# Optimization experiments

Measured on AMD Instinct MI355X. Metric: run time of the kernel, lower is better.

The kernel has to match this reference:

```python
import jax, jax.numpy as jnp
import numpy as np

N = 50000      # nodes
E = 800000     # edges (avg degree 16)
DIN = 128
HID = 128
OUT = 10       # classes
G = 64         # graphs in batch


def setup_inputs() -> dict:
    key = jax.random.key(0)
    ks = jax.random.split(key, 10)
    x = jax.random.normal(ks[0], (N, DIN), dtype=jnp.float32)
    edge_index = jax.random.randint(ks[1], (2, E), 0, N, dtype=jnp.int32)
    edge_weight = jax.random.uniform(ks[2], (E,), dtype=jnp.float32)
    batch = jnp.sort(jax.random.randint(ks[3], (N,), 0, G, dtype=jnp.int32))
    W1 = jax.random.normal(ks[4], (DIN, HID), dtype=jnp.float32) / np.sqrt(DIN)
    b1 = jnp.zeros((HID,), dtype=jnp.float32)
    W2 = jax.random.normal(ks[5], (HID, HID), dtype=jnp.float32) / np.sqrt(HID)
    b2 = jnp.zeros((HID,), dtype=jnp.float32)
    W3 = jax.random.normal(ks[6], (HID, OUT), dtype=jnp.float32) / np.sqrt(HID)
    b3 = jnp.zeros((OUT,), dtype=jnp.float32)
    return {"x": x, "edge_index": edge_index, "edge_weight": edge_weight,
            "batch": batch, "W1": W1, "b1": b1, "W2": W2, "b2": b2,
            "W3": W3, "b3": b3}


def _gcn_norm(edge_index, edge_weight, n_nodes):
    # PyG gcn_norm: add self-loops with weight 1, D^-1/2 (A+I) D^-1/2
    loop = jnp.arange(n_nodes, dtype=edge_index.dtype)
    src = jnp.concatenate([edge_index[0], loop])
    dst = jnp.concatenate([edge_index[1], loop])
    w = jnp.concatenate([edge_weight, jnp.ones((n_nodes,), edge_weight.dtype)])
    deg = jax.ops.segment_sum(w, dst, num_segments=n_nodes)
    dinv = jnp.where(deg > 0, jax.lax.rsqrt(deg), 0.0)
    norm = dinv[src] * w * dinv[dst]
    return src, dst, norm


def _gcn_conv(x, W, b, src, dst, norm, n_nodes):
    h = x @ W                                      # [N, F] dense transform
    msg = norm[:, None] * h[src]                   # gather + scale  [E+N, F]
    out = jax.ops.segment_sum(msg, dst, num_segments=n_nodes)  # scatter-add
    return out + b


def reference(x, edge_index, edge_weight, batch, W1, b1, W2, b2, W3, b3):
    src, dst, norm = _gcn_norm(edge_index, edge_weight, N)
    h = jax.nn.relu(_gcn_conv(x, W1, b1, src, dst, norm, N))
    h = jax.nn.relu(_gcn_conv(h, W2, b2, src, dst, norm, N))
    h = _gcn_conv(h, W3, b3, src, dst, norm, N)    # [N, OUT]
    # global_mean_pool over graph ids
    sums = jax.ops.segment_sum(h, batch, num_segments=G)          # [G, OUT]
    cnts = jax.ops.segment_sum(jnp.ones((N,), h.dtype), batch, num_segments=G)
    pooled = sums / jnp.maximum(cnts, 1.0)[:, None]
    return jax.nn.log_softmax(pooled, axis=1)
```

## Files before the change

### kernel.cpp

```cpp
#include <hip/hip_runtime.h>
#include <math.h>

#define NN 50000
#define EE 800000
#define GG 64
#define FD 128
#define OUTD 10
#define NB 49
#define GB 782
#define BB 196
#define NBU 196
#define NBK 128
#define CH 6250

typedef __attribute__((ext_vector_type(8))) short s8v;
typedef __attribute__((ext_vector_type(4))) float f4v;

static __device__ inline unsigned short f2b(float f) {
    unsigned int u = __float_as_uint(f);
    return (unsigned short)((u + 0x7FFFu + ((u >> 16) & 1u)) >> 16);
}


__global__ void k_prep(const float* __restrict__ W1, const float* __restrict__ W2,
                       unsigned short* __restrict__ Wt1, unsigned short* __restrict__ Wt2,
                       int* __restrict__ bflag) {
    int i = blockIdx.x * blockDim.x + threadIdx.x;
    if (i < FD * FD) {
        int nn = i >> 7, k = i & 127;
        Wt1[i] = f2b(W1[k * FD + nn]);
        Wt2[i] = f2b(W2[k * FD + nn]);
    }
    if (i < NB) bflag[i] = 0;
}


static __device__ inline void gemm_f32in_body(int bid, const float* __restrict__ A,
        const unsigned short* __restrict__ Wt, unsigned short* __restrict__ out, int n) {
    int tid = threadIdx.x;
    int wave = tid >> 6, lane = tid & 63;
    int quad = lane >> 4, c16 = lane & 15;
    int rowbase = bid * 64 + wave * 16;
    int rowA = rowbase + c16;
    if (rowA >= n) rowA = n - 1;
    f4v acc[8];
    #pragma unroll
    for (int t = 0; t < 8; ++t) acc[t] = (f4v){0.f, 0.f, 0.f, 0.f};
    #pragma unroll
    for (int k0 = 0; k0 < 128; k0 += 32) {
        const float* ap = A + (size_t)rowA * FD + k0 + quad * 8;
        float4 a0 = *(const float4*)ap;
        float4 a1 = *(const float4*)(ap + 4);
        s8v a;
        a[0] = (short)f2b(a0.x); a[1] = (short)f2b(a0.y);
        a[2] = (short)f2b(a0.z); a[3] = (short)f2b(a0.w);
        a[4] = (short)f2b(a1.x); a[5] = (short)f2b(a1.y);
        a[6] = (short)f2b(a1.z); a[7] = (short)f2b(a1.w);
        #pragma unroll
        for (int t = 0; t < 8; ++t) {
            s8v b = *(const s8v*)(Wt + (size_t)(t * 16 + c16) * FD + k0 + quad * 8);
            acc[t] = __builtin_amdgcn_mfma_f32_16x16x32_bf16(a, b, acc[t], 0, 0, 0);
        }
    }
    #pragma unroll
    for (int t = 0; t < 8; ++t) {
        #pragma unroll
        for (int r = 0; r < 4; ++r) {
            int row = rowbase + quad * 4 + r;
            if (row < n) out[(size_t)row * FD + t * 16 + c16] = f2b(acc[t][r]);
        }
    }
}

__global__ __launch_bounds__(256) void k_megaA(const float* __restrict__ x,
        const unsigned short* __restrict__ Wt1, unsigned short* __restrict__ hA,
        const int* __restrict__ dst, int* __restrict__ cnt2d,
        const int* __restrict__ batch, int* __restrict__ gstart) {
    int b = blockIdx.x;
    int tid = threadIdx.x;
    if (b < GB) {
        gemm_f32in_body(b, x, Wt1, hA, NN);
    } else if (b < GB + NBK) {
        __shared__ unsigned hist[NBU];
        int blk = b - GB;
        if (tid < NBU) hist[tid] = 0;
        __syncthreads();
        int e0 = blk * CH;
        for (int e = e0 + tid; e < e0 + CH; e += 256)
            atomicAdd(&hist[(unsigned)dst[e] >> 8], 1u);
        __syncthreads();
        if (tid < NBU) cnt2d[blk * NBU + tid] = (int)hist[tid];
    } else {
        int i = (b - GB - NBK) * 256 + tid;
        if (i < NN) {
            int bb = batch[i];
            int bp = (i == 0) ? -1 : batch[i - 1];
            for (int g = bp + 1; g <= bb; ++g) gstart[g] = i;
            if (i == NN - 1)
                for (int g = bb + 1; g <= GG; ++g) gstart[g] = NN;
        }
    }
}


__global__ __launch_bounds__(256) void k_bscan(int* __restrict__ cnt2d,
        int* __restrict__ bucketbase) {
    __shared__ int colsum[NBU];
    int tid = threadIdx.x;
    if (tid < NBU) {
        int run = 0;
        for (int blk = 0; blk < NBK; ++blk) {
            int idx = blk * NBU + tid;
            int t = cnt2d[idx];
            cnt2d[idx] = run;
            run += t;
        }
        colsum[tid] = run;
    }
    __syncthreads();
    if (tid == 0) {
        int run = 0;
        for (int b = 0; b < NBU; ++b) {
            bucketbase[b] = run;
            run += colsum[b];
        }
        bucketbase[NBU] = run;
    }
}


__global__ __launch_bounds__(256) void k_scatter(const int* __restrict__ src,
        const int* __restrict__ dst, const float* __restrict__ ew,
        const int* __restrict__ off2d, const int* __restrict__ bucketbase,
        uint2* __restrict__ rec) {
    __shared__ unsigned cur[NBU];
    int tid = threadIdx.x;
    int blk = blockIdx.x;
    if (tid < NBU) cur[tid] = (unsigned)(bucketbase[tid] + off2d[blk * NBU + tid]);
    __syncthreads();
    int e0 = blk * CH;
    for (int e = e0 + tid; e < e0 + CH; e += 256) {
        int d = dst[e];
        unsigned bkt = (unsigned)d >> 8;
        unsigned pos = atomicAdd(&cur[bkt], 1u);
        rec[pos] = make_uint2(((unsigned)(d & 255) << 16) | (unsigned)src[e],
                              __float_as_uint(ew[e]));
    }
}


__global__ __launch_bounds__(1024) void k_rank(const uint2* __restrict__ rec,
        const int* __restrict__ bucketbase, unsigned short* __restrict__ rankb,
        int* __restrict__ cnt_g, float* __restrict__ wdeg_g) {
    __shared__ unsigned cntS[256];
    __shared__ float wdegS[256];
    int b = blockIdx.x;
    int tid = threadIdx.x;
    if (tid < 256) { cntS[tid] = 0; wdegS[tid] = 0.0f; }
    __syncthreads();
    int beg = bucketbase[b], end = bucketbase[b + 1];
    for (int s = beg + tid; s < end; s += 1024) {
        uint2 r = rec[s];
        unsigned dl = r.x >> 16;
        unsigned old = atomicAdd(&cntS[dl], 1u);
        rankb[s] = (unsigned short)old;
        atomicAdd(&wdegS[dl], __uint_as_float(r.y));
    }
    __syncthreads();
    if (tid < 256) {
        int node = b * 256 + tid;
        if (node < NN) {
            cnt_g[node] = (int)cntS[tid];
            wdeg_g[node] = wdegS[tid];
        }
    }
}


__global__ __launch_bounds__(1024) void k_scan(const int* __restrict__ cnt_g,
        const float* __restrict__ wdeg_g, int* __restrict__ rowptr,
        float* __restrict__ dinv, uint2* __restrict__ ent,
        int* __restrict__ bsum, int* __restrict__ bflag, int n) {
    __shared__ int wtot[16];
    __shared__ int sbase_sh;
    int tid = threadIdx.x;
    int bid = blockIdx.x;
    int i = bid * 1024 + tid;
    int lane = tid & 63, wv = tid >> 6;

    int v_edges = 0, rowlen = 0;
    float di = 0.0f;
    if (i < n) {
        v_edges = cnt_g[i];
        float deg = wdeg_g[i] + 1.0f;
        di = 1.0f / sqrtf(deg);
        dinv[i] = di;
        rowlen = v_edges + 1;
    }
    int s = rowlen;
    #pragma unroll
    for (int off = 1; off < 64; off <<= 1) {
        int u = __shfl_up(s, off, 64);
        if (lane >= off) s += u;
    }
    if (lane == 63) wtot[wv] = s;
    __syncthreads();

    int btot = 0;
    #pragma unroll
    for (int j = 0; j < 16; ++j) btot += wtot[j];
    if (tid == 0) {
        bsum[bid] = btot;
        __hip_atomic_store(&bflag[bid], 1, __ATOMIC_RELEASE, __HIP_MEMORY_SCOPE_AGENT);
    }
    if (tid < 64) {
        int acc = 0;
        if (tid < bid) {
            while (__hip_atomic_load(&bflag[tid], __ATOMIC_ACQUIRE,
                                     __HIP_MEMORY_SCOPE_AGENT) == 0) {}
            acc = bsum[tid];
        }
        #pragma unroll
        for (int off = 32; off >= 1; off >>= 1) acc += __shfl_xor(acc, off, 64);
        if (tid == 0) sbase_sh = acc;
    }
    __syncthreads();
    int base = sbase_sh;

    int wpre = 0;
    for (int j = 0; j < wv; ++j) wpre += wtot[j];
    if (i < n) {
        int r = base + wpre + (s - rowlen);
        rowptr[i] = r;
        ent[r + v_edges] = make_uint2((unsigned)i, __float_as_uint(di * di));
    }
    if (bid == NB - 1 && tid == 0) rowptr[n] = base + btot;
}


__global__ __launch_bounds__(1024) void k_fill2(const uint2* __restrict__ rec,
        const unsigned short* __restrict__ rankb, const int* __restrict__ bucketbase,
        const int* __restrict__ rowptr, const float* __restrict__ dinv,
        uint2* __restrict__ ent) {
    int b = blockIdx.x;
    int tid = threadIdx.x;
    int beg = bucketbase[b], end = bucketbase[b + 1];
    for (int s = beg + tid; s < end; s += 1024) {
        uint2 r = rec[s];
        unsigned sn = r.x & 0xFFFFu;
        int d = (b << 8) | (int)(r.x >> 16);
        int pos = rowptr[d] + (int)rankb[s];
        float val = dinv[sn] * __uint_as_float(r.y) * dinv[d];
        ent[pos] = make_uint2(sn, __float_as_uint(val));
    }
}


__global__ __launch_bounds__(256) void k_gemm_bf(const unsigned short* __restrict__ A,
        const unsigned short* __restrict__ Wt, unsigned short* __restrict__ out, int n) {
    int tid = threadIdx.x;
    int wave = tid >> 6, lane = tid & 63;
    int quad = lane >> 4, c16 = lane & 15;
    int rowbase = blockIdx.x * 64 + wave * 16;
    int rowA = rowbase + c16;
    if (rowA >= n) rowA = n - 1;
    f4v acc[8];
    #pragma unroll
    for (int t = 0; t < 8; ++t) acc[t] = (f4v){0.f, 0.f, 0.f, 0.f};
    #pragma unroll
    for (int k0 = 0; k0 < 128; k0 += 32) {
        s8v a = *(const s8v*)(A + (size_t)rowA * FD + k0 + quad * 8);
        #pragma unroll
        for (int t = 0; t < 8; ++t) {
            s8v b = *(const s8v*)(Wt + (size_t)(t * 16 + c16) * FD + k0 + quad * 8);
            acc[t] = __builtin_amdgcn_mfma_f32_16x16x32_bf16(a, b, acc[t], 0, 0, 0);
        }
    }
    #pragma unroll
    for (int t = 0; t < 8; ++t) {
        #pragma unroll
        for (int r = 0; r < 4; ++r) {
            int row = rowbase + quad * 4 + r;
            if (row < n) out[(size_t)row * FD + t * 16 + c16] = f2b(acc[t][r]);
        }
    }
}

__global__ void k_gemm10(const unsigned short* __restrict__ A, const float* __restrict__ W,
                         float* __restrict__ out, int n) {
    __shared__ float Ws[FD * OUTD];
    int tid = threadIdx.x;
    for (int i = tid; i < FD * OUTD; i += blockDim.x) Ws[i] = W[i];
    __syncthreads();
    int i = blockIdx.x * blockDim.x + tid;
    if (i >= n) return;
    float acc[OUTD];
    #pragma unroll
    for (int c = 0; c < OUTD; ++c) acc[c] = 0.0f;
    const unsigned short* a = A + (size_t)i * FD;
    for (int k0 = 0; k0 < FD; k0 += 8) {
        uint4 t = *(const uint4*)(a + k0);
        float av[8];
        av[0] = __uint_as_float(t.x << 16); av[1] = __uint_as_float(t.x & 0xFFFF0000u);
        av[2] = __uint_as_float(t.y << 16); av[3] = __uint_as_float(t.y & 0xFFFF0000u);
        av[4] = __uint_as_float(t.z << 16); av[5] = __uint_as_float(t.z & 0xFFFF0000u);
        av[6] = __uint_as_float(t.w << 16); av[7] = __uint_as_float(t.w & 0xFFFF0000u);
        #pragma unroll
        for (int j = 0; j < 8; ++j)
            #pragma unroll
            for (int c = 0; c < OUTD; ++c) acc[c] += av[j] * Ws[(k0 + j) * OUTD + c];
    }
    float* o = out + (size_t)i * OUTD;
    #pragma unroll
    for (int c = 0; c < OUTD; ++c) o[c] = acc[c];
}

__global__ __launch_bounds__(256) void k_spmm_bf(const int* __restrict__ rowptr,
        const uint2* __restrict__ ent, const unsigned short* __restrict__ tin,
        const float* __restrict__ bias, unsigned short* __restrict__ out,
        int n, int dorelu) {
    int w = (blockIdx.x * blockDim.x + threadIdx.x) >> 6;
    int lane = threadIdx.x & 63;
    if (w >= n) return;
    int c = lane & 15, g = lane >> 4;
    int beg = rowptr[w], end = rowptr[w + 1];
    float acc[8];
    #pragma unroll
    for (int j = 0; j < 8; ++j) acc[j] = 0.0f;
    for (int e0 = beg; e0 < end; e0 += 16) {
        uint2 en[4];
        uint4 t[4];
        #pragma unroll
        for (int u = 0; u < 4; ++u) {
            int e = e0 + 4 * u + g;
            en[u] = (e < end) ? ent[e] : make_uint2(0u, 0u);
        }
        #pragma unroll
        for (int u = 0; u < 4; ++u)
            t[u] = *(const uint4*)(tin + (size_t)en[u].x * FD + c * 8);
        #pragma unroll
        for (int u = 0; u < 4; ++u) {
            float v = __uint_as_float(en[u].y);
            acc[0] += v * __uint_as_float(t[u].x << 16);
            acc[1] += v * __uint_as_float(t[u].x & 0xFFFF0000u);
            acc[2] += v * __uint_as_float(t[u].y << 16);
            acc[3] += v * __uint_as_float(t[u].y & 0xFFFF0000u);
            acc[4] += v * __uint_as_float(t[u].z << 16);
            acc[5] += v * __uint_as_float(t[u].z & 0xFFFF0000u);
            acc[6] += v * __uint_as_float(t[u].w << 16);
            acc[7] += v * __uint_as_float(t[u].w & 0xFFFF0000u);
        }
    }
    #pragma unroll
    for (int j = 0; j < 8; ++j) {
        acc[j] += __shfl_xor(acc[j], 16, 64);
        acc[j] += __shfl_xor(acc[j], 32, 64);
    }
    if (g == 0) {
        uint4 r;
        float o[8];
        #pragma unroll
        for (int j = 0; j < 8; ++j) {
            float x = acc[j] + bias[c * 8 + j];
            o[j] = dorelu ? fmaxf(x, 0.0f) : x;
        }
        r.x = (unsigned)f2b(o[0]) | ((unsigned)f2b(o[1]) << 16);
        r.y = (unsigned)f2b(o[2]) | ((unsigned)f2b(o[3]) << 16);
        r.z = (unsigned)f2b(o[4]) | ((unsigned)f2b(o[5]) << 16);
        r.w = (unsigned)f2b(o[6]) | ((unsigned)f2b(o[7]) << 16);
        *(uint4*)(out + (size_t)w * FD + c * 8) = r;
    }
}

__global__ void k_spmm10(const int* __restrict__ rowptr, const uint2* __restrict__ ent,
        const float* __restrict__ tin, const float* __restrict__ bias,
        float* __restrict__ out, int n) {
    int t = blockIdx.x * blockDim.x + threadIdx.x;
    int node = t / OUTD;
    int c = t - node * OUTD;
    if (node >= n) return;
    int beg = rowptr[node], end = rowptr[node + 1];
    float acc = 0.0f;
    for (int e = beg; e < end; ++e) {
        uint2 en = ent[e];
        acc += __uint_as_float(en.y) * tin[(size_t)en.x * OUTD + c];
    }
    out[(size_t)node * OUTD + c] = acc + bias[c];
}


__global__ __launch_bounds__(256) void k_poolfin(const float* __restrict__ h,
        const int* __restrict__ gstart, float* __restrict__ out) {
    int g = blockIdx.x;
    int beg = gstart[g], end = gstart[g + 1];
    int tid = threadIdx.x;
    int lane = tid & 63, wv = tid >> 6;
    float acc[OUTD];
    #pragma unroll
    for (int c = 0; c < OUTD; ++c) acc[c] = 0.0f;
    for (int i = beg + tid; i < end; i += 256) {
        const float* hp = h + (size_t)i * OUTD;
        #pragma unroll
        for (int c = 0; c < OUTD; ++c) acc[c] += hp[c];
    }
    #pragma unroll
    for (int off = 32; off >= 1; off >>= 1)
        #pragma unroll
        for (int c = 0; c < OUTD; ++c) acc[c] += __shfl_down(acc[c], off, 64);
    __shared__ float ws[4][OUTD];
    if (lane == 0)
        #pragma unroll
        for (int c = 0; c < OUTD; ++c) ws[wv][c] = acc[c];
    __syncthreads();
    if (tid == 0) {
        float cf = fmaxf((float)(end - beg), 1.0f);
        float v[OUTD], m = -1e30f;
        #pragma unroll
        for (int c = 0; c < OUTD; ++c) {
            v[c] = (ws[0][c] + ws[1][c] + ws[2][c] + ws[3][c]) / cf;
            m = fmaxf(m, v[c]);
        }
        float s = 0.0f;
        #pragma unroll
        for (int c = 0; c < OUTD; ++c) s += expf(v[c] - m);
        float l = logf(s);
        #pragma unroll
        for (int c = 0; c < OUTD; ++c) out[g * OUTD + c] = v[c] - m - l;
    }
}


extern "C" void kernel_launch(void* const* d_in, const int* in_sizes, int n_in,
                              void* d_out, int out_size, void* d_ws, size_t ws_size,
                              hipStream_t stream) {
    const float* x   = (const float*)d_in[0];
    const int*   ei  = (const int*)d_in[1];
    const float* ew  = (const float*)d_in[2];
    const int*   bat = (const int*)d_in[3];
    const float* W1  = (const float*)d_in[4];
    const float* b1  = (const float*)d_in[5];
    const float* W2  = (const float*)d_in[6];
    const float* b2  = (const float*)d_in[7];
    const float* W3  = (const float*)d_in[8];
    const float* b3  = (const float*)d_in[9];
    float* out = (float*)d_out;

    const int* src = ei;
    const int* dst = ei + EE;

    char* p = (char*)d_ws;
    auto alloc = [&](size_t bytes) -> void* {
        void* r = (void*)p;
        p += (bytes + 255) & ~(size_t)255;
        return r;
    };
    int*            cnt2d  = (int*)  alloc((size_t)NBK * NBU * 4);
    int*            bbase  = (int*)  alloc((size_t)(NBU + 1) * 4);
    uint2*          rec    = (uint2*)alloc((size_t)EE * 8);
    unsigned short* rankb  = (unsigned short*)alloc((size_t)EE * 2);
    int*            cnt_g  = (int*)  alloc((size_t)NN * 4);
    float*          wdeg_g = (float*)alloc((size_t)NN * 4);
    float*          dinv   = (float*)alloc((size_t)NN * 4);
    int*            rowptr = (int*)  alloc((size_t)(NN + 1) * 4);
    uint2*          ent    = (uint2*)alloc((size_t)(EE + NN) * 8);
    unsigned short* Wt1    = (unsigned short*)alloc((size_t)FD * FD * 2);
    unsigned short* Wt2    = (unsigned short*)alloc((size_t)FD * FD * 2);
    unsigned short* hA     = (unsigned short*)alloc((size_t)NN * FD * 2);
    unsigned short* hB     = (unsigned short*)alloc((size_t)NN * FD * 2);
    float*          bufC   = (float*)alloc((size_t)NN * OUTD * 4);
    float*          bufD   = (float*)alloc((size_t)NN * OUTD * 4);
    int*            bsum   = (int*)  alloc((size_t)NB * 4);
    int*            bflag  = (int*)  alloc((size_t)NB * 4);
    int*            gstart = (int*)  alloc((size_t)(GG + 1) * 4);
    (void)ws_size; (void)in_sizes; (void)n_in; (void)out_size;

    const int B = 256;
    k_prep   <<<(FD * FD + B - 1) / B, B, 0, stream>>>(W1, W2, Wt1, Wt2, bflag);
    k_megaA  <<<GB + NBK + BB, B, 0, stream>>>(x, Wt1, hA, dst, cnt2d, bat, gstart);
    k_bscan  <<<1, B, 0, stream>>>(cnt2d, bbase);
    k_scatter<<<NBK, B, 0, stream>>>(src, dst, ew, cnt2d, bbase, rec);
    k_rank   <<<NBU, 1024, 0, stream>>>(rec, bbase, rankb, cnt_g, wdeg_g);
    k_scan   <<<NB, 1024, 0, stream>>>(cnt_g, wdeg_g, rowptr, dinv, ent, bsum, bflag, NN);
    k_fill2  <<<NBU, 1024, 0, stream>>>(rec, rankb, bbase, rowptr, dinv, ent);

    k_spmm_bf<<<(NN * 64 + B - 1) / B, B, 0, stream>>>(rowptr, ent, hA, b1, hB, NN, 1);
    k_gemm_bf<<<GB, B, 0, stream>>>(hB, Wt2, hA, NN);
    k_spmm_bf<<<(NN * 64 + B - 1) / B, B, 0, stream>>>(rowptr, ent, hA, b2, hB, NN, 1);
    k_gemm10 <<<(NN + B - 1) / B, B, 0, stream>>>(hB, W3, bufC, NN);
    k_spmm10 <<<(NN * OUTD + B - 1) / B, B, 0, stream>>>(rowptr, ent, bufC, b3, bufD, NN);
    k_poolfin<<<GG, 256, 0, stream>>>(bufD, gstart, out);
}
```

Measured before the change: 281.8 us.

## Fold bucket scan into scatter and row scan into rank kernel

```diff
diff --git a/kernel.cpp b/kernel.cpp
--- a/kernel.cpp
+++ b/kernel.cpp
@@ -6,7 +6,6 @@
 #define GG 64
 #define FD 128
 #define OUTD 10
-#define NB 49
 #define GB 782
 #define BB 196
 #define NBU 196
@@ -23,15 +22,13 @@
 
 
 __global__ void k_prep(const float* __restrict__ W1, const float* __restrict__ W2,
-                       unsigned short* __restrict__ Wt1, unsigned short* __restrict__ Wt2,
-                       int* __restrict__ bflag) {
+                       unsigned short* __restrict__ Wt1, unsigned short* __restrict__ Wt2) {
     int i = blockIdx.x * blockDim.x + threadIdx.x;
     if (i < FD * FD) {
         int nn = i >> 7, k = i & 127;
         Wt1[i] = f2b(W1[k * FD + nn]);
         Wt2[i] = f2b(W2[k * FD + nn]);
     }
-    if (i < NB) bflag[i] = 0;
 }
 
 
@@ -89,7 +86,7 @@
         for (int e = e0 + tid; e < e0 + CH; e += 256)
             atomicAdd(&hist[(unsigned)dst[e] >> 8], 1u);
         __syncthreads();
-        if (tid < NBU) cnt2d[blk * NBU + tid] = (int)hist[tid];
+        if (tid < NBU) cnt2d[tid * NBK + blk] = (int)hist[tid];
     } else {
         int i = (b - GB - NBK) * 256 + tid;
         if (i < NN) {
@@ -103,40 +100,48 @@
 }
 
 
-__global__ __launch_bounds__(256) void k_bscan(int* __restrict__ cnt2d,
-        int* __restrict__ bucketbase) {
-    __shared__ int colsum[NBU];
-    int tid = threadIdx.x;
-    if (tid < NBU) {
-        int run = 0;
-        for (int blk = 0; blk < NBK; ++blk) {
-            int idx = blk * NBU + tid;
-            int t = cnt2d[idx];
-            cnt2d[idx] = run;
-            run += t;
-        }
-        colsum[tid] = run;
-    }
-    __syncthreads();
-    if (tid == 0) {
-        int run = 0;
-        for (int b = 0; b < NBU; ++b) {
-            bucketbase[b] = run;
-            run += colsum[b];
-        }
-        bucketbase[NBU] = run;
-    }
-}
-
-
 __global__ __launch_bounds__(256) void k_scatter(const int* __restrict__ src,
         const int* __restrict__ dst, const float* __restrict__ ew,
-        const int* __restrict__ off2d, const int* __restrict__ bucketbase,
+        const int* __restrict__ cnt2d, int* __restrict__ bbase_g,
         uint2* __restrict__ rec) {
+    __shared__ int colsum[NBU];
+    __shared__ int ownoff[NBU];
     __shared__ unsigned cur[NBU];
+    __shared__ int wtot_s[4];
     int tid = threadIdx.x;
     int blk = blockIdx.x;
-    if (tid < NBU) cur[tid] = (unsigned)(bucketbase[tid] + off2d[blk * NBU + tid]);
+    if (tid < NBU) {
+        const int* c = cnt2d + tid * NBK;
+        int own = 0, tot = 0;
+        for (int b = 0; b < NBK; ++b) {
+            int t = c[b];
+            if (b < blk) own += t;
+            tot += t;
+        }
+        ownoff[tid] = own;
+        colsum[tid] = tot;
+    }
+    __syncthreads();
+    {
+        int lane = tid & 63, wv = tid >> 6;
+        int v = (tid < NBU) ? colsum[tid] : 0;
+        int s = v;
+        #pragma unroll
+        for (int off = 1; off < 64; off <<= 1) {
+            int u = __shfl_up(s, off, 64);
+            if (lane >= off) s += u;
+        }
+        if (lane == 63) wtot_s[wv] = s;
+        __syncthreads();
+        int pre = 0;
+        for (int j = 0; j < wv; ++j) pre += wtot_s[j];
+        int base = pre + s - v;
+        if (tid < NBU) {
+            cur[tid] = (unsigned)(base + ownoff[tid]);
+            if (blk == 0) bbase_g[tid] = base;
+        }
+        if (blk == 0 && tid == NBU - 1) bbase_g[NBU] = base + v;
+    }
     __syncthreads();
     int e0 = blk * CH;
     for (int e = e0 + tid; e < e0 + CH; e += 256) {
@@ -150,15 +155,16 @@
 
 
 __global__ __launch_bounds__(1024) void k_rank(const uint2* __restrict__ rec,
-        const int* __restrict__ bucketbase, unsigned short* __restrict__ rankb,
-        int* __restrict__ cnt_g, float* __restrict__ wdeg_g) {
+        const int* __restrict__ bbase, unsigned short* __restrict__ rankb,
+        int* __restrict__ rowptr, float* __restrict__ dinv, uint2* __restrict__ ent) {
     __shared__ unsigned cntS[256];
     __shared__ float wdegS[256];
+    __shared__ int wtot_s[4];
     int b = blockIdx.x;
     int tid = threadIdx.x;
     if (tid < 256) { cntS[tid] = 0; wdegS[tid] = 0.0f; }
     __syncthreads();
-    int beg = bucketbase[b], end = bucketbase[b + 1];
+    int beg = bbase[b], end = bbase[b + 1];
     for (int s = beg + tid; s < end; s += 1024) {
         uint2 r = rec[s];
         unsigned dl = r.x >> 16;
@@ -168,83 +174,39 @@
     }
     __syncthreads();
     if (tid < 256) {
+        int lane = tid & 63, wv = tid >> 6;
+        int v = (int)cntS[tid];
+        int s = v;
+        #pragma unroll
+        for (int off = 1; off < 64; off <<= 1) {
+            int u = __shfl_up(s, off, 64);
+            if (lane >= off) s += u;
+        }
+        if (lane == 63) wtot_s[wv] = s;
+        __syncthreads();
+        int pre = 0;
+        for (int j = 0; j < wv; ++j) pre += wtot_s[j];
+        int excl = pre + s - v;
         int node = b * 256 + tid;
         if (node < NN) {
-            cnt_g[node] = (int)cntS[tid];
-            wdeg_g[node] = wdegS[tid];
-        }
-    }
-}
-
-
-__global__ __launch_bounds__(1024) void k_scan(const int* __restrict__ cnt_g,
-        const float* __restrict__ wdeg_g, int* __restrict__ rowptr,
-        float* __restrict__ dinv, uint2* __restrict__ ent,
-        int* __restrict__ bsum, int* __restrict__ bflag, int n) {
-    __shared__ int wtot[16];
-    __shared__ int sbase_sh;
-    int tid = threadIdx.x;
-    int bid = blockIdx.x;
-    int i = bid * 1024 + tid;
-    int lane = tid & 63, wv = tid >> 6;
-
-    int v_edges = 0, rowlen = 0;
-    float di = 0.0f;
-    if (i < n) {
-        v_edges = cnt_g[i];
-        float deg = wdeg_g[i] + 1.0f;
-        di = 1.0f / sqrtf(deg);
-        dinv[i] = di;
-        rowlen = v_edges + 1;
-    }
-    int s = rowlen;
-    #pragma unroll
-    for (int off = 1; off < 64; off <<= 1) {
-        int u = __shfl_up(s, off, 64);
-        if (lane >= off) s += u;
-    }
-    if (lane == 63) wtot[wv] = s;
-    __syncthreads();
-
-    int btot = 0;
-    #pragma unroll
-    for (int j = 0; j < 16; ++j) btot += wtot[j];
-    if (tid == 0) {
-        bsum[bid] = btot;
-        __hip_atomic_store(&bflag[bid], 1, __ATOMIC_RELEASE, __HIP_MEMORY_SCOPE_AGENT);
-    }
-    if (tid < 64) {
-        int acc = 0;
-        if (tid < bid) {
-            while (__hip_atomic_load(&bflag[tid], __ATOMIC_ACQUIRE,
-                                     __HIP_MEMORY_SCOPE_AGENT) == 0) {}
-            acc = bsum[tid];
-        }
-        #pragma unroll
-        for (int off = 32; off >= 1; off >>= 1) acc += __shfl_xor(acc, off, 64);
-        if (tid == 0) sbase_sh = acc;
-    }
-    __syncthreads();
-    int base = sbase_sh;
-
-    int wpre = 0;
-    for (int j = 0; j < wv; ++j) wpre += wtot[j];
-    if (i < n) {
-        int r = base + wpre + (s - rowlen);
-        rowptr[i] = r;
-        ent[r + v_edges] = make_uint2((unsigned)i, __float_as_uint(di * di));
-    }
-    if (bid == NB - 1 && tid == 0) rowptr[n] = base + btot;
+            int r = beg + node + excl;
+            rowptr[node] = r;
+            float di = 1.0f / sqrtf(wdegS[tid] + 1.0f);
+            dinv[node] = di;
+            ent[r + v] = make_uint2((unsigned)node, __float_as_uint(di * di));
+        }
+        if (node == NN - 1) rowptr[NN] = EE + NN;
+    }
 }
 
 
 __global__ __launch_bounds__(1024) void k_fill2(const uint2* __restrict__ rec,
-        const unsigned short* __restrict__ rankb, const int* __restrict__ bucketbase,
+        const unsigned short* __restrict__ rankb, const int* __restrict__ bbase,
         const int* __restrict__ rowptr, const float* __restrict__ dinv,
         uint2* __restrict__ ent) {
     int b = blockIdx.x;
     int tid = threadIdx.x;
-    int beg = bucketbase[b], end = bucketbase[b + 1];
+    int beg = bbase[b], end = bbase[b + 1];
     for (int s = beg + tid; s < end; s += 1024) {
         uint2 r = rec[s];
         unsigned sn = r.x & 0xFFFFu;
@@ -327,14 +289,12 @@
     float acc[8];
     #pragma unroll
     for (int j = 0; j < 8; ++j) acc[j] = 0.0f;
-    for (int e0 = beg; e0 < end; e0 += 16) {
+    int e0 = beg;
+    for (; e0 + 16 <= end; e0 += 16) {
         uint2 en[4];
         uint4 t[4];
         #pragma unroll
-        for (int u = 0; u < 4; ++u) {
-            int e = e0 + 4 * u + g;
-            en[u] = (e < end) ? ent[e] : make_uint2(0u, 0u);
-        }
+        for (int u = 0; u < 4; ++u) en[u] = ent[e0 + 4 * u + g];
         #pragma unroll
         for (int u = 0; u < 4; ++u)
             t[u] = *(const uint4*)(tin + (size_t)en[u].x * FD + c * 8);
@@ -350,6 +310,20 @@
             acc[6] += v * __uint_as_float(t[u].w << 16);
             acc[7] += v * __uint_as_float(t[u].w & 0xFFFF0000u);
         }
+    }
+    for (; e0 < end; e0 += 4) {
+        int e = e0 + g;
+        uint2 en = (e < end) ? ent[e] : make_uint2(0u, 0u);
+        float v = (e < end) ? __uint_as_float(en.y) : 0.0f;
+        uint4 t = *(const uint4*)(tin + (size_t)en.x * FD + c * 8);
+        acc[0] += v * __uint_as_float(t.x << 16);
+        acc[1] += v * __uint_as_float(t.x & 0xFFFF0000u);
+        acc[2] += v * __uint_as_float(t.y << 16);
+        acc[3] += v * __uint_as_float(t.y & 0xFFFF0000u);
+        acc[4] += v * __uint_as_float(t.z << 16);
+        acc[5] += v * __uint_as_float(t.z & 0xFFFF0000u);
+        acc[6] += v * __uint_as_float(t.w << 16);
+        acc[7] += v * __uint_as_float(t.w & 0xFFFF0000u);
     }
     #pragma unroll
     for (int j = 0; j < 8; ++j) {
@@ -454,12 +428,10 @@
         p += (bytes + 255) & ~(size_t)255;
         return r;
     };
-    int*            cnt2d  = (int*)  alloc((size_t)NBK * NBU * 4);
+    int*            cnt2d  = (int*)  alloc((size_t)NBU * NBK * 4);
     int*            bbase  = (int*)  alloc((size_t)(NBU + 1) * 4);
     uint2*          rec    = (uint2*)alloc((size_t)EE * 8);
     unsigned short* rankb  = (unsigned short*)alloc((size_t)EE * 2);
-    int*            cnt_g  = (int*)  alloc((size_t)NN * 4);
-    float*          wdeg_g = (float*)alloc((size_t)NN * 4);
     float*          dinv   = (float*)alloc((size_t)NN * 4);
     int*            rowptr = (int*)  alloc((size_t)(NN + 1) * 4);
     uint2*          ent    = (uint2*)alloc((size_t)(EE + NN) * 8);
@@ -469,18 +441,14 @@
     unsigned short* hB     = (unsigned short*)alloc((size_t)NN * FD * 2);
     float*          bufC   = (float*)alloc((size_t)NN * OUTD * 4);
     float*          bufD   = (float*)alloc((size_t)NN * OUTD * 4);
-    int*            bsum   = (int*)  alloc((size_t)NB * 4);
-    int*            bflag  = (int*)  alloc((size_t)NB * 4);
     int*            gstart = (int*)  alloc((size_t)(GG + 1) * 4);
     (void)ws_size; (void)in_sizes; (void)n_in; (void)out_size;
 
     const int B = 256;
-    k_prep   <<<(FD * FD + B - 1) / B, B, 0, stream>>>(W1, W2, Wt1, Wt2, bflag);
+    k_prep   <<<(FD * FD + B - 1) / B, B, 0, stream>>>(W1, W2, Wt1, Wt2);
     k_megaA  <<<GB + NBK + BB, B, 0, stream>>>(x, Wt1, hA, dst, cnt2d, bat, gstart);
-    k_bscan  <<<1, B, 0, stream>>>(cnt2d, bbase);
     k_scatter<<<NBK, B, 0, stream>>>(src, dst, ew, cnt2d, bbase, rec);
-    k_rank   <<<NBU, 1024, 0, stream>>>(rec, bbase, rankb, cnt_g, wdeg_g);
-    k_scan   <<<NB, 1024, 0, stream>>>(cnt_g, wdeg_g, rowptr, dinv, ent, bsum, bflag, NN);
+    k_rank   <<<NBU, 1024, 0, stream>>>(rec, bbase, rankb, rowptr, dinv, ent);
     k_fill2  <<<NBU, 1024, 0, stream>>>(rec, rankb, bbase, rowptr, dinv, ent);
 
     k_spmm_bf<<<(NN * 64 + B - 1) / B, B, 0, stream>>>(rowptr, ent, hA, b1, hB, NN, 1);
```

After: 268.2 us. -4.8%, faster.
